# Kernel tuning notes

Hardware: AMD Instinct MI355X
Metric: run time of the kernel (lower is better)

The kernel has to match this reference:

```python
import jax, jax.numpy as jnp
import numpy as np

N_NODES = 100000
N_EDGES = 1600000
N_GRAPHS = 2048
D = 128
H = 128
EPS = 1e-5


def gcn_conv(x, src, dst, W, b, n):
    # x: [N, Din], W: [Din, Dout]; GCN with added self-loops and symmetric norm
    xw = x @ W                                       # [N, Dout]
    deg = jnp.zeros((n,), x.dtype).at[dst].add(1.0) + 1.0  # deg of A+I (counted on dst)
    dinv = jax.lax.rsqrt(deg)                        # [N]
    norm = dinv[src] * dinv[dst]                     # [E]
    msg = xw[src] * norm[:, None]                    # [E, Dout] gather + scale
    agg = jax.ops.segment_sum(msg, dst, num_segments=n)
    agg = agg + xw * (dinv * dinv)[:, None]          # self-loop contribution
    return agg + b


def gru_step_h0(x, W_ih, W_hh, b_ih, b_hh):
    # single GRU step with h0 = 0 (PyTorch gate order r, z, n)
    h0 = jnp.zeros_like(x)
    gi = x @ W_ih.T + b_ih                           # [G, 3H]
    gh = h0 @ W_hh.T + b_hh                          # [G, 3H] (zeros + b_hh)
    ir, iz, inn = jnp.split(gi, 3, axis=-1)
    hr, hz, hn = jnp.split(gh, 3, axis=-1)
    r = jax.nn.sigmoid(ir + hr)
    z = jax.nn.sigmoid(iz + hz)
    n = jnp.tanh(inn + r * hn)
    return (1.0 - z) * n + z * h0


def setup_inputs() -> dict:
    key = jax.random.key(0)
    ks = jax.random.split(key, 10)
    x = jax.random.normal(ks[0], (N_NODES, D), jnp.float32)
    edge_index = jax.random.randint(ks[1], (2, N_EDGES), 0, N_NODES, jnp.int32)
    batch = jnp.sort(jax.random.randint(ks[2], (N_NODES,), 0, N_GRAPHS, jnp.int32))
    s = 1.0 / np.sqrt(H)
    return {
        "x": x,
        "edge_index": edge_index,
        "batch": batch,
        "W1": jax.random.normal(ks[3], (D, H), jnp.float32) * s,
        "b1": jnp.zeros((H,), jnp.float32),
        "W2": jax.random.normal(ks[4], (H, H), jnp.float32) * s,
        "b2": jnp.zeros((H,), jnp.float32),
        "W_ih": jax.random.normal(ks[5], (3 * H, H), jnp.float32) * s,
        "W_hh": jax.random.normal(ks[6], (3 * H, H), jnp.float32) * s,
        "b_ih": jnp.zeros((3 * H,), jnp.float32),
        "b_hh": jnp.zeros((3 * H,), jnp.float32),
        "W_lin": jax.random.normal(ks[7], (1, H), jnp.float32) * s,
        "b_lin": jnp.zeros((1,), jnp.float32),
    }


def reference(x, edge_index, batch, W1, b1, W2, b2, W_ih, W_hh, b_ih, b_hh, W_lin, b_lin):
    src, dst = edge_index[0], edge_index[1]
    n = x.shape[0]
    h = jax.nn.relu(gcn_conv(x, src, dst, W1, b1, n))
    h = gcn_conv(h, src, dst, W2, b2, n)
    # global_mean_pool over graph ids
    sums = jax.ops.segment_sum(h, batch, num_segments=N_GRAPHS)
    cnts = jax.ops.segment_sum(jnp.ones((n,), h.dtype), batch, num_segments=N_GRAPHS)
    g = sums / jnp.maximum(cnts, 1.0)[:, None]       # [G, H]
    # dropout p=0.5 in eval mode -> identity
    g = gru_step_h0(g, W_ih, W_hh, b_ih, b_hh)
    g = jax.nn.relu(g)
    mu = jnp.mean(g, axis=-1, keepdims=True)
    var = jnp.mean(jnp.square(g - mu), axis=-1, keepdims=True)
    g = (g - mu) * jax.lax.rsqrt(var + EPS)          # layer_norm, no affine
    return g @ W_lin.T + b_lin                       # [G, 1]
```

## Files before the change

kernel.cpp:

```cpp
#include <hip/hip_runtime.h>
#include <hip/hip_bf16.h>
#include <math.h>

#define DHID 128
#define SH 8
#define BIN_T 8192
#define CAPSH 13
#define SRC_SH 13

typedef __attribute__((ext_vector_type(8))) short bf16x8;
typedef __attribute__((ext_vector_type(4))) float f32x4;

__device__ __forceinline__ int atomAddI(int* p, int v) {
    return __hip_atomic_fetch_add(p, v, __ATOMIC_RELAXED, __HIP_MEMORY_SCOPE_AGENT);
}
__device__ __forceinline__ float bf_lo(unsigned u) { return __uint_as_float(u << 16); }
__device__ __forceinline__ float bf_hi(unsigned u) { return __uint_as_float(u & 0xffff0000u); }
__device__ __forceinline__ float bf_us(unsigned short u) { return __uint_as_float((unsigned)u << 16); }
__device__ __forceinline__ unsigned short bf16_1(float f) {
    unsigned u = __float_as_uint(f);
    u += 0x7fffu + ((u >> 16) & 1u);
    return (unsigned short)(u >> 16);
}
__device__ __forceinline__ unsigned pack_bf16x2(float a, float b) {
    unsigned ua = __float_as_uint(a);
    unsigned ub = __float_as_uint(b);
    ua = (ua + 0x7fffu + ((ua >> 16) & 1u)) >> 16;
    ub = (ub + 0x7fffu + ((ub >> 16) & 1u)) & 0xffff0000u;
    return ua | ub;
}

__global__ __launch_bounds__(256) void bin_edges(const int* __restrict__ src,
                                                 const int* __restrict__ dst,
                                                 int* __restrict__ bcur,
                                                 unsigned* __restrict__ staged,
                                                 const float* __restrict__ W1,
                                                 const float* __restrict__ W2,
                                                 const float* __restrict__ Wih,
                                                 unsigned short* __restrict__ Wt1,
                                                 unsigned short* __restrict__ Wt2,
                                                 unsigned short* __restrict__ Wihb,
                                                 int E, int NB, int nb_bin) {
    int t = threadIdx.x;
    if (blockIdx.x >= nb_bin) {
        int idx = (blockIdx.x - nb_bin) * 256 + t;
        if (idx < 16384) {
            int k = idx >> 7, n = idx & 127;
            Wt1[n * 128 + k] = bf16_1(W1[idx]);
        } else if (idx < 32768) {
            int j = idx - 16384;
            int k = j >> 7, n = j & 127;
            Wt2[n * 128 + k] = bf16_1(W2[j]);
        } else if (idx < 32768 + 49152) {
            int j = idx - 32768;
            Wihb[j] = bf16_1(Wih[j]);
        }
        return;
    }
    __shared__ int lh[512], lbase[512], lcur[512];
    int e0 = blockIdx.x * BIN_T;
    int eend = min(e0 + BIN_T, E);
    for (int i = t; i < NB; i += 256) { lh[i] = 0; lcur[i] = 0; }
    __syncthreads();
    for (int e = e0 + t; e < eend; e += 256)
        atomicAdd(&lh[dst[e] >> SH], 1);
    __syncthreads();
    for (int i = t; i < NB; i += 256)
        lbase[i] = lh[i] ? atomAddI(&bcur[i], lh[i]) : 0;
    __syncthreads();
    for (int e = e0 + t; e < eend; e += 256) {
        int d = dst[e];
        int b = d >> SH;
        int pos = lbase[b] + atomicAdd(&lcur[b], 1);
        staged[((size_t)b << CAPSH) + pos] =
            (unsigned)src[e] | ((unsigned)(d & ((1 << SH) - 1)) << 24);
    }
}

__global__ __launch_bounds__(256) void scatter_csr(const unsigned* __restrict__ staged,
                                                   const int* __restrict__ bcur,
                                                   int* __restrict__ off,
                                                   float* __restrict__ dinv,
                                                   int* __restrict__ rec,
                                                   int N, int E, int NB) {
    __shared__ int hist[4096];
    __shared__ int sh[256];
    int t = threadIdx.x;
    int b = blockIdx.x;
    int node0 = b << SH;

    int s0 = (t < b) ? bcur[t] : 0;
    int s1 = (256 + t < b) ? bcur[256 + t] : 0;
    int s = s0 + s1;
#pragma unroll
    for (int o = 1; o < 64; o <<= 1) s += __shfl_xor(s, o);
    if ((t & 63) == 0) sh[t >> 6] = s;
    __syncthreads();
    int base = sh[0] + sh[1] + sh[2] + sh[3];
    __syncthreads();

    for (int i = t; i < 4096; i += 256) hist[i] = 0;
    __syncthreads();
    int cnt_b = bcur[b];
    const unsigned* st = staged + ((size_t)b << CAPSH);
    for (int j = t; j < cnt_b; j += 256) {
        unsigned w = st[j];
        int key = (int)((w >> 24) << 4) | (int)((w & 0xFFFFFFu) >> SRC_SH);
        atomicAdd(&hist[key], 1);
    }
    __syncthreads();

    int loc[16];
    int run = 0;
    int base16 = t * 16;
#pragma unroll
    for (int i = 0; i < 16; i++) { loc[i] = run; run += hist[base16 + i]; }
    sh[t] = run;
    __syncthreads();
#pragma unroll
    for (int o = 1; o < 256; o <<= 1) {
        int x = (t >= o) ? sh[t - o] : 0;
        __syncthreads();
        sh[t] += x;
        __syncthreads();
    }
    int excl = sh[t] - run;
#pragma unroll
    for (int i = 0; i < 16; i++) hist[base16 + i] = base + excl + loc[i];

    int node = node0 + t;
    if (node < N) {
        off[node] = base + excl;
        dinv[node] = rsqrtf((float)run + 1.0f);
    }
    if (b == NB - 1 && t == 0) off[N] = E;
    __syncthreads();

    for (int j = t; j < cnt_b; j += 256) {
        unsigned w = st[j];
        int key = (int)((w >> 24) << 4) | (int)((w & 0xFFFFFFu) >> SRC_SH);
        int pos = atomicAdd(&hist[key], 1);
        rec[pos] = (int)(w & 0xFFFFFFu);
    }
}

__global__ __launch_bounds__(256) void gemm_mfma(const void* __restrict__ Xv,
                                                 const unsigned short* __restrict__ Wt,
                                                 unsigned short* __restrict__ Y,
                                                 int N, int x_is_bf16,
                                                 int wstride, int ystride) {
    __shared__ unsigned short Xs[64 * 136];
    __shared__ unsigned short Ws[128 * 136];
    const int tid = threadIdx.x;
    const unsigned short* Wg = Wt + (size_t)blockIdx.y * wstride;
    unsigned short* Yg = Y + (size_t)blockIdx.y * ystride;

    {
        const uint4* W4 = (const uint4*)Wg;
#pragma unroll
        for (int i = 0; i < 8; i++) {
            int idx = tid + i * 256;
            int r = idx >> 4, c8 = idx & 15;
            *(uint4*)&Ws[r * 136 + c8 * 8] = W4[idx];
        }
    }
    const int row0 = blockIdx.x * 64;
    if (x_is_bf16) {
        const uint4* X4 = (const uint4*)Xv;
#pragma unroll
        for (int i = 0; i < 4; i++) {
            int idx = tid + i * 256;
            int r = idx >> 4, c8 = idx & 15;
            uint4 v = make_uint4(0u, 0u, 0u, 0u);
            if (row0 + r < N) v = X4[(size_t)(row0 + r) * 16 + c8];
            *(uint4*)&Xs[r * 136 + c8 * 8] = v;
        }
    } else {
        const float4* X4 = (const float4*)Xv;
#pragma unroll
        for (int i = 0; i < 8; i++) {
            int idx = tid + i * 256;
            int r = idx >> 5, c4 = idx & 31;
            float4 v = make_float4(0.f, 0.f, 0.f, 0.f);
            if (row0 + r < N) v = X4[(size_t)(row0 + r) * 32 + c4];
            uint2 pk = make_uint2(pack_bf16x2(v.x, v.y), pack_bf16x2(v.z, v.w));
            *(uint2*)&Xs[r * 136 + c4 * 4] = pk;
        }
    }
    __syncthreads();

    const int lane = tid & 63;
    const int wv = tid >> 6;
    const int m = lane & 15, quad = lane >> 4;
    const int wrow = wv * 16;

    f32x4 acc[8];
#pragma unroll
    for (int i = 0; i < 8; i++) acc[i] = (f32x4){0.f, 0.f, 0.f, 0.f};

#pragma unroll
    for (int kc = 0; kc < 4; kc++) {
        bf16x8 a = *(const bf16x8*)&Xs[(wrow + m) * 136 + kc * 32 + quad * 8];
#pragma unroll
        for (int nt = 0; nt < 8; nt++) {
            bf16x8 b = *(const bf16x8*)&Ws[(nt * 16 + m) * 136 + kc * 32 + quad * 8];
            acc[nt] = __builtin_amdgcn_mfma_f32_16x16x32_bf16(a, b, acc[nt], 0, 0, 0);
        }
    }

#pragma unroll
    for (int r = 0; r < 4; r++) {
        int lrow = wrow + quad * 4 + r;
#pragma unroll
        for (int nt = 0; nt < 8; nt++)
            Xs[lrow * 136 + nt * 16 + m] = bf16_1(acc[nt][r]);
    }
    __syncthreads();
#pragma unroll
    for (int i = 0; i < 4; i++) {
        int idx = tid + i * 256;
        int r = idx >> 4, c8 = idx & 15;
        if (row0 + r < N)
            *(uint4*)&Yg[(size_t)(row0 + r) * DHID + c8 * 8] =
                *(const uint4*)&Xs[r * 136 + c8 * 8];
    }
}

__global__ __launch_bounds__(256) void aggregate(const unsigned short* __restrict__ A,
                                                 const float* __restrict__ dinv,
                                                 const int* __restrict__ off,
                                                 const int* __restrict__ rec,
                                                 const float* __restrict__ bias,
                                                 unsigned short* __restrict__ Bout,
                                                 int N, int mode) {
    int node = blockIdx.x * 4 + (threadIdx.x >> 6);
    if (node >= N) return;
    int lane = threadIdx.x & 63;
    int q  = lane >> 4;
    int ql = lane & 15;
    float di = dinv[node];
    float2 acc[4];
    if (q == 0) {
        float s = di * di;
        uint4 v = ((const uint4*)(A + (size_t)node * DHID))[ql];
        const float4* bb = (const float4*)(bias + ql * 8);
        float4 b0 = bb[0], b1 = bb[1];
        acc[0] = make_float2(bf_lo(v.x) * s + b0.x, bf_hi(v.x) * s + b0.y);
        acc[1] = make_float2(bf_lo(v.y) * s + b0.z, bf_hi(v.y) * s + b0.w);
        acc[2] = make_float2(bf_lo(v.z) * s + b1.x, bf_hi(v.z) * s + b1.y);
        acc[3] = make_float2(bf_lo(v.w) * s + b1.z, bf_hi(v.w) * s + b1.w);
    } else {
#pragma unroll
        for (int i = 0; i < 4; i++) acc[i] = make_float2(0.f, 0.f);
    }
    int j = off[node] + q;
    int jend = off[node + 1];
    if (j + 4 < jend) {
        int s0 = rec[j], s1 = rec[j + 4];
        for (; j + 12 < jend; j += 8) {
            int n0 = rec[j + 8], n1 = rec[j + 12];
            uint4 v0 = ((const uint4*)(A + (size_t)s0 * DHID))[ql];
            uint4 v1 = ((const uint4*)(A + (size_t)s1 * DHID))[ql];
            float w0 = dinv[s0] * di;
            float w1 = dinv[s1] * di;
            acc[0].x += bf_lo(v0.x) * w0 + bf_lo(v1.x) * w1;
            acc[0].y += bf_hi(v0.x) * w0 + bf_hi(v1.x) * w1;
            acc[1].x += bf_lo(v0.y) * w0 + bf_lo(v1.y) * w1;
            acc[1].y += bf_hi(v0.y) * w0 + bf_hi(v1.y) * w1;
            acc[2].x += bf_lo(v0.z) * w0 + bf_lo(v1.z) * w1;
            acc[2].y += bf_hi(v0.z) * w0 + bf_hi(v1.z) * w1;
            acc[3].x += bf_lo(v0.w) * w0 + bf_lo(v1.w) * w1;
            acc[3].y += bf_hi(v0.w) * w0 + bf_hi(v1.w) * w1;
            s0 = n0; s1 = n1;
        }
        {
            uint4 v0 = ((const uint4*)(A + (size_t)s0 * DHID))[ql];
            uint4 v1 = ((const uint4*)(A + (size_t)s1 * DHID))[ql];
            float w0 = dinv[s0] * di;
            float w1 = dinv[s1] * di;
            acc[0].x += bf_lo(v0.x) * w0 + bf_lo(v1.x) * w1;
            acc[0].y += bf_hi(v0.x) * w0 + bf_hi(v1.x) * w1;
            acc[1].x += bf_lo(v0.y) * w0 + bf_lo(v1.y) * w1;
            acc[1].y += bf_hi(v0.y) * w0 + bf_hi(v1.y) * w1;
            acc[2].x += bf_lo(v0.z) * w0 + bf_lo(v1.z) * w1;
            acc[2].y += bf_hi(v0.z) * w0 + bf_hi(v1.z) * w1;
            acc[3].x += bf_lo(v0.w) * w0 + bf_lo(v1.w) * w1;
            acc[3].y += bf_hi(v0.w) * w0 + bf_hi(v1.w) * w1;
            j += 8;
        }
    }
    if (j < jend) {
        int s0 = rec[j];
        uint4 v0 = ((const uint4*)(A + (size_t)s0 * DHID))[ql];
        float w0 = dinv[s0] * di;
        acc[0].x += bf_lo(v0.x) * w0;
        acc[0].y += bf_hi(v0.x) * w0;
        acc[1].x += bf_lo(v0.y) * w0;
        acc[1].y += bf_hi(v0.y) * w0;
        acc[2].x += bf_lo(v0.z) * w0;
        acc[2].y += bf_hi(v0.z) * w0;
        acc[3].x += bf_lo(v0.w) * w0;
        acc[3].y += bf_hi(v0.w) * w0;
    }
#pragma unroll
    for (int i = 0; i < 4; i++) {
        acc[i].x += __shfl_xor(acc[i].x, 16);
        acc[i].y += __shfl_xor(acc[i].y, 16);
        acc[i].x += __shfl_xor(acc[i].x, 32);
        acc[i].y += __shfl_xor(acc[i].y, 32);
    }
    if (q == 0) {
        if (mode == 1) {
#pragma unroll
            for (int i = 0; i < 4; i++) {
                acc[i].x = fmaxf(acc[i].x, 0.f);
                acc[i].y = fmaxf(acc[i].y, 0.f);
            }
        }
        uint4 pk;
        pk.x = pack_bf16x2(acc[0].x, acc[0].y);
        pk.y = pack_bf16x2(acc[1].x, acc[1].y);
        pk.z = pack_bf16x2(acc[2].x, acc[2].y);
        pk.w = pack_bf16x2(acc[3].x, acc[3].y);
        ((uint4*)(Bout + (size_t)node * DHID))[ql] = pk;
    }
}

__global__ __launch_bounds__(256) void pool_mean(const unsigned short* __restrict__ B,
                                                 const int* __restrict__ batch,
                                                 float* __restrict__ g, int N, int G) {
    __shared__ int se[2];
    __shared__ float red[128];
    const int t = threadIdx.x;
    const int gr = blockIdx.x;
    if (t < 2) {
        int target = gr + t, lo = 0, hi = N;
        while (lo < hi) {
            int mid = (lo + hi) >> 1;
            if (batch[mid] < target) lo = mid + 1; else hi = mid;
        }
        se[t] = lo;
    }
    __syncthreads();
    const int s = se[0], e = se[1];
    const int col = t & 127, rh = t >> 7;
    float sum = 0.f;
    for (int r = s + rh; r < e; r += 2) sum += bf_us(B[(size_t)r * DHID + col]);
    if (rh == 1) red[col] = sum;
    __syncthreads();
    if (rh == 0) {
        float tot = sum + red[col];
        g[(size_t)gr * DHID + col] = tot / fmaxf((float)(e - s), 1.0f);
    }
}

__global__ __launch_bounds__(128) void gate_ln_head(const unsigned short* __restrict__ gi,
                                                    const float* __restrict__ b_ih,
                                                    const float* __restrict__ b_hh,
                                                    const float* __restrict__ W_lin,
                                                    const float* __restrict__ b_lin,
                                                    float* __restrict__ out, int G) {
    __shared__ float red[2];
    const int t = threadIdx.x;
    const int g = blockIdx.x;

    float d0 = bf_us(gi[(size_t)g * DHID + t]);
    float d1 = bf_us(gi[(size_t)(G + g) * DHID + t]);
    float d2 = bf_us(gi[(size_t)(2 * G + g) * DHID + t]);

    float rg = 1.f / (1.f + expf(-(d0 + b_ih[t] + b_hh[t])));
    float zg = 1.f / (1.f + expf(-(d1 + b_ih[128 + t] + b_hh[128 + t])));
    float ng = tanhf(d2 + b_ih[256 + t] + rg * b_hh[256 + t]);
    float y = fmaxf((1.f - zg) * ng, 0.f);

    auto blockSum = [&](float v) -> float {
#pragma unroll
        for (int o = 1; o < 64; o <<= 1) v += __shfl_xor(v, o);
        __syncthreads();
        if ((t & 63) == 0) red[t >> 6] = v;
        __syncthreads();
        return red[0] + red[1];
    };

    float mu = blockSum(y) * (1.f / 128.f);
    float dy = y - mu;
    float var = blockSum(dy * dy) * (1.f / 128.f);
    float yn = dy * rsqrtf(var + 1e-5f);
    float tot = blockSum(yn * W_lin[t]);
    if (t == 0) out[g] = tot + b_lin[0];
}

extern "C" void kernel_launch(void* const* d_in, const int* in_sizes, int n_in,
                              void* d_out, int out_size, void* d_ws, size_t ws_size,
                              hipStream_t stream) {
    const float* x     = (const float*)d_in[0];
    const int*   ei    = (const int*)d_in[1];
    const int*   batch = (const int*)d_in[2];
    const float* W1    = (const float*)d_in[3];
    const float* b1    = (const float*)d_in[4];
    const float* W2    = (const float*)d_in[5];
    const float* b2    = (const float*)d_in[6];
    const float* W_ih  = (const float*)d_in[7];
    const float* b_ih  = (const float*)d_in[9];
    const float* b_hh  = (const float*)d_in[10];
    const float* W_lin = (const float*)d_in[11];
    const float* b_lin = (const float*)d_in[12];
    float* out = (float*)d_out;

    const int N = in_sizes[0] / DHID;
    const int E = in_sizes[1] / 2;
    const int G = out_size;
    const int* src = ei;
    const int* dst = ei + E;
    const int NB = (N + (1 << SH) - 1) >> SH;

    auto align256 = [](size_t v) { return (v + 255) & ~(size_t)255; };
    char* p = (char*)d_ws;
    size_t used = 0;
    auto carve = [&](size_t bytes) -> char* {
        char* q = p + used;
        used += align256(bytes);
        return q;
    };

    int*   off    = (int*)carve(((size_t)N + 1) * 4);
    int*   bcur   = (int*)carve(512 * 4);
    float* dinv   = (float*)carve((size_t)N * 4);
    unsigned* staged = (unsigned*)carve(((size_t)NB << CAPSH) * 4);
    int*   rec    = (int*)carve((size_t)E * 4);
    float* gbuf   = (float*)carve((size_t)G * DHID * 4);
    unsigned short* Wt1  = (unsigned short*)carve((size_t)128 * 128 * 2);
    unsigned short* Wt2  = (unsigned short*)carve((size_t)128 * 128 * 2);
    unsigned short* Wihb = (unsigned short*)carve((size_t)3 * 128 * 128 * 2);
    unsigned short* gib  = (unsigned short*)carve((size_t)3 * G * DHID * 2);
    unsigned short* A    = (unsigned short*)carve((size_t)N * DHID * 2);
    unsigned short* B1b  = (unsigned short*)carve((size_t)N * DHID * 2);
    size_t matB = (size_t)N * DHID * 2;
    unsigned short* B2b;
    if (ws_size >= used + matB) {
        B2b = (unsigned short*)carve(matB);
    } else {
        B2b = (unsigned short*)d_in[0];
    }

    dim3 blk(256);
    int nb_g  = (N + 63) / 64;
    int nb_ag = (N + 3) / 4;
    int nb_bin = (E + BIN_T - 1) / BIN_T;
    int nb_wp  = (81920 + 255) / 256;

    hipMemsetAsync(bcur, 0, (size_t)NB * 4, stream);
    bin_edges<<<nb_bin + nb_wp, blk, 0, stream>>>(src, dst, bcur, staged,
                                                  W1, W2, W_ih, Wt1, Wt2, Wihb,
                                                  E, NB, nb_bin);
    scatter_csr<<<NB, blk, 0, stream>>>(staged, bcur, off, dinv, rec, N, E, NB);

    gemm_mfma<<<dim3(nb_g, 1), blk, 0, stream>>>(x, Wt1, A, N, 0, 0, 0);
    aggregate<<<nb_ag, blk, 0, stream>>>(A, dinv, off, rec, b1, B1b, N, 1);

    gemm_mfma<<<dim3(nb_g, 1), blk, 0, stream>>>(B1b, Wt2, A, N, 1, 0, 0);
    aggregate<<<nb_ag, blk, 0, stream>>>(A, dinv, off, rec, b2, B2b, N, 0);

    pool_mean<<<G, blk, 0, stream>>>(B2b, batch, gbuf, N, G);
    gemm_mfma<<<dim3((G + 63) / 64, 3), blk, 0, stream>>>(gbuf, Wihb, gib, G, 0,
                                                          128 * 128, G * DHID);
    gate_ln_head<<<G, dim3(128), 0, stream>>>(gib, b_ih, b_hh, W_lin, b_lin, out, G);
}
```

Baseline: 348.7 us.

## Merge CSR scatter with first GEMM into one launch; deepen aggregate gather unroll

Folds the CSR scatter blocks and the first-layer x@W1 GEMM blocks into a single kernel, branching on block index, so both independent stages run concurrently and one launch is removed. The aggregate kernel's edge loop now issues four row gathers per iteration instead of a software-pipelined pair, giving more memory-level parallelism. The fused kernel carries the larger of the two shared-memory footprints (about 51 KB) for every block, which may limit occupancy for the scatter blocks. The wider unroll also raises register use in aggregate.

Measured after the change: 336.8 us. -3.4%, faster.

```diff
diff --git a/kernel.cpp b/kernel.cpp
--- a/kernel.cpp
+++ b/kernel.cpp
@@ -77,152 +77,139 @@
     }
 }
 
-__global__ __launch_bounds__(256) void scatter_csr(const unsigned* __restrict__ staged,
-                                                   const int* __restrict__ bcur,
-                                                   int* __restrict__ off,
-                                                   float* __restrict__ dinv,
-                                                   int* __restrict__ rec,
-                                                   int N, int E, int NB) {
-    __shared__ int hist[4096];
-    __shared__ int sh[256];
-    int t = threadIdx.x;
-    int b = blockIdx.x;
-    int node0 = b << SH;
-
-    int s0 = (t < b) ? bcur[t] : 0;
-    int s1 = (256 + t < b) ? bcur[256 + t] : 0;
-    int s = s0 + s1;
-#pragma unroll
-    for (int o = 1; o < 64; o <<= 1) s += __shfl_xor(s, o);
-    if ((t & 63) == 0) sh[t >> 6] = s;
-    __syncthreads();
-    int base = sh[0] + sh[1] + sh[2] + sh[3];
-    __syncthreads();
-
-    for (int i = t; i < 4096; i += 256) hist[i] = 0;
-    __syncthreads();
-    int cnt_b = bcur[b];
-    const unsigned* st = staged + ((size_t)b << CAPSH);
-    for (int j = t; j < cnt_b; j += 256) {
-        unsigned w = st[j];
-        int key = (int)((w >> 24) << 4) | (int)((w & 0xFFFFFFu) >> SRC_SH);
-        atomicAdd(&hist[key], 1);
-    }
-    __syncthreads();
-
-    int loc[16];
-    int run = 0;
-    int base16 = t * 16;
-#pragma unroll
-    for (int i = 0; i < 16; i++) { loc[i] = run; run += hist[base16 + i]; }
-    sh[t] = run;
-    __syncthreads();
-#pragma unroll
-    for (int o = 1; o < 256; o <<= 1) {
-        int x = (t >= o) ? sh[t - o] : 0;
-        __syncthreads();
-        sh[t] += x;
-        __syncthreads();
-    }
-    int excl = sh[t] - run;
-#pragma unroll
-    for (int i = 0; i < 16; i++) hist[base16 + i] = base + excl + loc[i];
-
-    int node = node0 + t;
-    if (node < N) {
-        off[node] = base + excl;
-        dinv[node] = rsqrtf((float)run + 1.0f);
-    }
-    if (b == NB - 1 && t == 0) off[N] = E;
-    __syncthreads();
-
-    for (int j = t; j < cnt_b; j += 256) {
-        unsigned w = st[j];
-        int key = (int)((w >> 24) << 4) | (int)((w & 0xFFFFFFu) >> SRC_SH);
-        int pos = atomicAdd(&hist[key], 1);
-        rec[pos] = (int)(w & 0xFFFFFFu);
-    }
-}
-
-__global__ __launch_bounds__(256) void gemm_mfma(const void* __restrict__ Xv,
-                                                 const unsigned short* __restrict__ Wt,
-                                                 unsigned short* __restrict__ Y,
-                                                 int N, int x_is_bf16,
-                                                 int wstride, int ystride) {
-    __shared__ unsigned short Xs[64 * 136];
-    __shared__ unsigned short Ws[128 * 136];
+__global__ __launch_bounds__(256) void scatter_gemm(const unsigned* __restrict__ staged,
+                                                    const int* __restrict__ bcur,
+                                                    int* __restrict__ off,
+                                                    float* __restrict__ dinv,
+                                                    int* __restrict__ rec,
+                                                    int N, int E, int NB,
+                                                    const float* __restrict__ Xf,
+                                                    const unsigned short* __restrict__ Wt,
+                                                    unsigned short* __restrict__ Y) {
+    __shared__ __align__(16) unsigned char smem[52224];
     const int tid = threadIdx.x;
-    const unsigned short* Wg = Wt + (size_t)blockIdx.y * wstride;
-    unsigned short* Yg = Y + (size_t)blockIdx.y * ystride;
-
-    {
-        const uint4* W4 = (const uint4*)Wg;
-#pragma unroll
-        for (int i = 0; i < 8; i++) {
-            int idx = tid + i * 256;
-            int r = idx >> 4, c8 = idx & 15;
-            *(uint4*)&Ws[r * 136 + c8 * 8] = W4[idx];
-        }
-    }
-    const int row0 = blockIdx.x * 64;
-    if (x_is_bf16) {
-        const uint4* X4 = (const uint4*)Xv;
+    if (blockIdx.x < NB) {
+        int* hist = (int*)smem;
+        int* sh   = (int*)(smem + 16384);
+        int t = tid;
+        int b = blockIdx.x;
+        int node0 = b << SH;
+
+        int s0 = (t < b) ? bcur[t] : 0;
+        int s1 = (256 + t < b) ? bcur[256 + t] : 0;
+        int s = s0 + s1;
+#pragma unroll
+        for (int o = 1; o < 64; o <<= 1) s += __shfl_xor(s, o);
+        if ((t & 63) == 0) sh[t >> 6] = s;
+        __syncthreads();
+        int base = sh[0] + sh[1] + sh[2] + sh[3];
+        __syncthreads();
+
+        for (int i = t; i < 4096; i += 256) hist[i] = 0;
+        __syncthreads();
+        int cnt_b = bcur[b];
+        const unsigned* st = staged + ((size_t)b << CAPSH);
+        for (int j = t; j < cnt_b; j += 256) {
+            unsigned w = st[j];
+            int key = (int)((w >> 24) << 4) | (int)((w & 0xFFFFFFu) >> SRC_SH);
+            atomicAdd(&hist[key], 1);
+        }
+        __syncthreads();
+
+        int loc[16];
+        int run = 0;
+        int base16 = t * 16;
+#pragma unroll
+        for (int i = 0; i < 16; i++) { loc[i] = run; run += hist[base16 + i]; }
+        sh[t] = run;
+        __syncthreads();
+#pragma unroll
+        for (int o = 1; o < 256; o <<= 1) {
+            int x = (t >= o) ? sh[t - o] : 0;
+            __syncthreads();
+            sh[t] += x;
+            __syncthreads();
+        }
+        int excl = sh[t] - run;
+#pragma unroll
+        for (int i = 0; i < 16; i++) hist[base16 + i] = base + excl + loc[i];
+
+        int node = node0 + t;
+        if (node < N) {
+            off[node] = base + excl;
+            dinv[node] = rsqrtf((float)run + 1.0f);
+        }
+        if (b == NB - 1 && t == 0) off[N] = E;
+        __syncthreads();
+
+        for (int j = t; j < cnt_b; j += 256) {
+            unsigned w = st[j];
+            int key = (int)((w >> 24) << 4) | (int)((w & 0xFFFFFFu) >> SRC_SH);
+            int pos = atomicAdd(&hist[key], 1);
+            rec[pos] = (int)(w & 0xFFFFFFu);
+        }
+    } else {
+        unsigned short* Xs = (unsigned short*)smem;
+        unsigned short* Ws = (unsigned short*)(smem + 17408);
+        {
+            const uint4* W4 = (const uint4*)Wt;
+#pragma unroll
+            for (int i = 0; i < 8; i++) {
+                int idx = tid + i * 256;
+                int r = idx >> 4, c8 = idx & 15;
+                *(uint4*)&Ws[r * 136 + c8 * 8] = W4[idx];
+            }
+        }
+        const int row0 = (blockIdx.x - NB) * 64;
+        {
+            const float4* X4 = (const float4*)Xf;
+#pragma unroll
+            for (int i = 0; i < 8; i++) {
+                int idx = tid + i * 256;
+                int r = idx >> 5, c4 = idx & 31;
+                float4 v = make_float4(0.f, 0.f, 0.f, 0.f);
+                if (row0 + r < N) v = X4[(size_t)(row0 + r) * 32 + c4];
+                uint2 pk = make_uint2(pack_bf16x2(v.x, v.y), pack_bf16x2(v.z, v.w));
+                *(uint2*)&Xs[r * 136 + c4 * 4] = pk;
+            }
+        }
+        __syncthreads();
+
+        const int lane = tid & 63;
+        const int wv = tid >> 6;
+        const int m = lane & 15, quad = lane >> 4;
+        const int wrow = wv * 16;
+
+        f32x4 acc[8];
+#pragma unroll
+        for (int i = 0; i < 8; i++) acc[i] = (f32x4){0.f, 0.f, 0.f, 0.f};
+
+#pragma unroll
+        for (int kc = 0; kc < 4; kc++) {
+            bf16x8 a = *(const bf16x8*)&Xs[(wrow + m) * 136 + kc * 32 + quad * 8];
+#pragma unroll
+            for (int nt = 0; nt < 8; nt++) {
+                bf16x8 bfr = *(const bf16x8*)&Ws[(nt * 16 + m) * 136 + kc * 32 + quad * 8];
+                acc[nt] = __builtin_amdgcn_mfma_f32_16x16x32_bf16(a, bfr, acc[nt], 0, 0, 0);
+            }
+        }
+
+#pragma unroll
+        for (int r = 0; r < 4; r++) {
+            int lrow = wrow + quad * 4 + r;
+#pragma unroll
+            for (int nt = 0; nt < 8; nt++)
+                Xs[lrow * 136 + nt * 16 + m] = bf16_1(acc[nt][r]);
+        }
+        __syncthreads();
 #pragma unroll
         for (int i = 0; i < 4; i++) {
             int idx = tid + i * 256;
             int r = idx >> 4, c8 = idx & 15;
-            uint4 v = make_uint4(0u, 0u, 0u, 0u);
-            if (row0 + r < N) v = X4[(size_t)(row0 + r) * 16 + c8];
-            *(uint4*)&Xs[r * 136 + c8 * 8] = v;
-        }
-    } else {
-        const float4* X4 = (const float4*)Xv;
-#pragma unroll
-        for (int i = 0; i < 8; i++) {
-            int idx = tid + i * 256;
-            int r = idx >> 5, c4 = idx & 31;
-            float4 v = make_float4(0.f, 0.f, 0.f, 0.f);
-            if (row0 + r < N) v = X4[(size_t)(row0 + r) * 32 + c4];
-            uint2 pk = make_uint2(pack_bf16x2(v.x, v.y), pack_bf16x2(v.z, v.w));
-            *(uint2*)&Xs[r * 136 + c4 * 4] = pk;
-        }
-    }
-    __syncthreads();
-
-    const int lane = tid & 63;
-    const int wv = tid >> 6;
-    const int m = lane & 15, quad = lane >> 4;
-    const int wrow = wv * 16;
-
-    f32x4 acc[8];
-#pragma unroll
-    for (int i = 0; i < 8; i++) acc[i] = (f32x4){0.f, 0.f, 0.f, 0.f};
-
-#pragma unroll
-    for (int kc = 0; kc < 4; kc++) {
-        bf16x8 a = *(const bf16x8*)&Xs[(wrow + m) * 136 + kc * 32 + quad * 8];
-#pragma unroll
-        for (int nt = 0; nt < 8; nt++) {
-            bf16x8 b = *(const bf16x8*)&Ws[(nt * 16 + m) * 136 + kc * 32 + quad * 8];
-            acc[nt] = __builtin_amdgcn_mfma_f32_16x16x32_bf16(a, b, acc[nt], 0, 0, 0);
-        }
-    }
-
-#pragma unroll
-    for (int r = 0; r < 4; r++) {
-        int lrow = wrow + quad * 4 + r;
-#pragma unroll
-        for (int nt = 0; nt < 8; nt++)
-            Xs[lrow * 136 + nt * 16 + m] = bf16_1(acc[nt][r]);
-    }
-    __syncthreads();
-#pragma unroll
-    for (int i = 0; i < 4; i++) {
-        int idx = tid + i * 256;
-        int r = idx >> 4, c8 = idx & 15;
-        if (row0 + r < N)
-            *(uint4*)&Yg[(size_t)(row0 + r) * DHID + c8 * 8] =
-                *(const uint4*)&Xs[r * 136 + c8 * 8];
+            if (row0 + r < N)
+                *(uint4*)&Y[(size_t)(row0 + r) * DHID + c8 * 8] =
+                    *(const uint4*)&Xs[r * 136 + c8 * 8];
+        }
     }
 }
 
@@ -255,39 +242,39 @@
     }
     int j = off[node] + q;
     int jend = off[node + 1];
-    if (j + 4 < jend) {
+    for (; j + 12 < jend; j += 16) {
+        int s0 = rec[j], s1 = rec[j + 4], s2 = rec[j + 8], s3 = rec[j + 12];
+        uint4 v0 = ((const uint4*)(A + (size_t)s0 * DHID))[ql];
+        uint4 v1 = ((const uint4*)(A + (size_t)s1 * DHID))[ql];
+        uint4 v2 = ((const uint4*)(A + (size_t)s2 * DHID))[ql];
+        uint4 v3 = ((const uint4*)(A + (size_t)s3 * DHID))[ql];
+        float w0 = dinv[s0] * di;
+        float w1 = dinv[s1] * di;
+        float w2 = dinv[s2] * di;
+        float w3 = dinv[s3] * di;
+        acc[0].x += bf_lo(v0.x) * w0 + bf_lo(v1.x) * w1 + bf_lo(v2.x) * w2 + bf_lo(v3.x) * w3;
+        acc[0].y += bf_hi(v0.x) * w0 + bf_hi(v1.x) * w1 + bf_hi(v2.x) * w2 + bf_hi(v3.x) * w3;
+        acc[1].x += bf_lo(v0.y) * w0 + bf_lo(v1.y) * w1 + bf_lo(v2.y) * w2 + bf_lo(v3.y) * w3;
+        acc[1].y += bf_hi(v0.y) * w0 + bf_hi(v1.y) * w1 + bf_hi(v2.y) * w2 + bf_hi(v3.y) * w3;
+        acc[2].x += bf_lo(v0.z) * w0 + bf_lo(v1.z) * w1 + bf_lo(v2.z) * w2 + bf_lo(v3.z) * w3;
+        acc[2].y += bf_hi(v0.z) * w0 + bf_hi(v1.z) * w1 + bf_hi(v2.z) * w2 + bf_hi(v3.z) * w3;
+        acc[3].x += bf_lo(v0.w) * w0 + bf_lo(v1.w) * w1 + bf_lo(v2.w) * w2 + bf_lo(v3.w) * w3;
+        acc[3].y += bf_hi(v0.w) * w0 + bf_hi(v1.w) * w1 + bf_hi(v2.w) * w2 + bf_hi(v3.w) * w3;
+    }
+    for (; j + 4 < jend; j += 8) {
         int s0 = rec[j], s1 = rec[j + 4];
-        for (; j + 12 < jend; j += 8) {
-            int n0 = rec[j + 8], n1 = rec[j + 12];
-            uint4 v0 = ((const uint4*)(A + (size_t)s0 * DHID))[ql];
-            uint4 v1 = ((const uint4*)(A + (size_t)s1 * DHID))[ql];
-            float w0 = dinv[s0] * di;
-            float w1 = dinv[s1] * di;
-            acc[0].x += bf_lo(v0.x) * w0 + bf_lo(v1.x) * w1;
-            acc[0].y += bf_hi(v0.x) * w0 + bf_hi(v1.x) * w1;
-            acc[1].x += bf_lo(v0.y) * w0 + bf_lo(v1.y) * w1;
-            acc[1].y += bf_hi(v0.y) * w0 + bf_hi(v1.y) * w1;
-            acc[2].x += bf_lo(v0.z) * w0 + bf_lo(v1.z) * w1;
-            acc[2].y += bf_hi(v0.z) * w0 + bf_hi(v1.z) * w1;
-            acc[3].x += bf_lo(v0.w) * w0 + bf_lo(v1.w) * w1;
-            acc[3].y += bf_hi(v0.w) * w0 + bf_hi(v1.w) * w1;
-            s0 = n0; s1 = n1;
-        }
-        {
-            uint4 v0 = ((const uint4*)(A + (size_t)s0 * DHID))[ql];
-            uint4 v1 = ((const uint4*)(A + (size_t)s1 * DHID))[ql];
-            float w0 = dinv[s0] * di;
-            float w1 = dinv[s1] * di;
-            acc[0].x += bf_lo(v0.x) * w0 + bf_lo(v1.x) * w1;
-            acc[0].y += bf_hi(v0.x) * w0 + bf_hi(v1.x) * w1;
-            acc[1].x += bf_lo(v0.y) * w0 + bf_lo(v1.y) * w1;
-            acc[1].y += bf_hi(v0.y) * w0 + bf_hi(v1.y) * w1;
-            acc[2].x += bf_lo(v0.z) * w0 + bf_lo(v1.z) * w1;
-            acc[2].y += bf_hi(v0.z) * w0 + bf_hi(v1.z) * w1;
-            acc[3].x += bf_lo(v0.w) * w0 + bf_lo(v1.w) * w1;
-            acc[3].y += bf_hi(v0.w) * w0 + bf_hi(v1.w) * w1;
-            j += 8;
-        }
+        uint4 v0 = ((const uint4*)(A + (size_t)s0 * DHID))[ql];
+        uint4 v1 = ((const uint4*)(A + (size_t)s1 * DHID))[ql];
+        float w0 = dinv[s0] * di;
+        float w1 = dinv[s1] * di;
+        acc[0].x += bf_lo(v0.x) * w0 + bf_lo(v1.x) * w1;
+        acc[0].y += bf_hi(v0.x) * w0 + bf_hi(v1.x) * w1;
+        acc[1].x += bf_lo(v0.y) * w0 + bf_lo(v1.y) * w1;
+        acc[1].y += bf_hi(v0.y) * w0 + bf_hi(v1.y) * w1;
+        acc[2].x += bf_lo(v0.z) * w0 + bf_lo(v1.z) * w1;
+        acc[2].y += bf_hi(v0.z) * w0 + bf_hi(v1.z) * w1;
+        acc[3].x += bf_lo(v0.w) * w0 + bf_lo(v1.w) * w1;
+        acc[3].y += bf_hi(v0.w) * w0 + bf_hi(v1.w) * w1;
     }
     if (j < jend) {
         int s0 = rec[j];
@@ -323,6 +310,88 @@
         pk.z = pack_bf16x2(acc[2].x, acc[2].y);
         pk.w = pack_bf16x2(acc[3].x, acc[3].y);
         ((uint4*)(Bout + (size_t)node * DHID))[ql] = pk;
+    }
+}
+
+__global__ __launch_bounds__(256) void gemm_mfma(const void* __restrict__ Xv,
+                                                 const unsigned short* __restrict__ Wt,
+                                                 unsigned short* __restrict__ Y,
+                                                 int N, int x_is_bf16,
+                                                 int wstride, int ystride) {
+    __shared__ unsigned short Xs[64 * 136];
+    __shared__ unsigned short Ws[128 * 136];
+    const int tid = threadIdx.x;
+    const unsigned short* Wg = Wt + (size_t)blockIdx.y * wstride;
+    unsigned short* Yg = Y + (size_t)blockIdx.y * ystride;
+
+    {
+        const uint4* W4 = (const uint4*)Wg;
+#pragma unroll
+        for (int i = 0; i < 8; i++) {
+            int idx = tid + i * 256;
+            int r = idx >> 4, c8 = idx & 15;
+            *(uint4*)&Ws[r * 136 + c8 * 8] = W4[idx];
+        }
+    }
+    const int row0 = blockIdx.x * 64;
+    if (x_is_bf16) {
+        const uint4* X4 = (const uint4*)Xv;
+#pragma unroll
+        for (int i = 0; i < 4; i++) {
+            int idx = tid + i * 256;
+            int r = idx >> 4, c8 = idx & 15;
+            uint4 v = make_uint4(0u, 0u, 0u, 0u);
+            if (row0 + r < N) v = X4[(size_t)(row0 + r) * 16 + c8];
+            *(uint4*)&Xs[r * 136 + c8 * 8] = v;
+        }
+    } else {
+        const float4* X4 = (const float4*)Xv;
+#pragma unroll
+        for (int i = 0; i < 8; i++) {
+            int idx = tid + i * 256;
+            int r = idx >> 5, c4 = idx & 31;
+            float4 v = make_float4(0.f, 0.f, 0.f, 0.f);
+            if (row0 + r < N) v = X4[(size_t)(row0 + r) * 32 + c4];
+            uint2 pk = make_uint2(pack_bf16x2(v.x, v.y), pack_bf16x2(v.z, v.w));
+            *(uint2*)&Xs[r * 136 + c4 * 4] = pk;
+        }
+    }
+    __syncthreads();
+
+    const int lane = tid & 63;
+    const int wv = tid >> 6;
+    const int m = lane & 15, quad = lane >> 4;
+    const int wrow = wv * 16;
+
+    f32x4 acc[8];
+#pragma unroll
+    for (int i = 0; i < 8; i++) acc[i] = (f32x4){0.f, 0.f, 0.f, 0.f};
+
+#pragma unroll
+    for (int kc = 0; kc < 4; kc++) {
+        bf16x8 a = *(const bf16x8*)&Xs[(wrow + m) * 136 + kc * 32 + quad * 8];
+#pragma unroll
+        for (int nt = 0; nt < 8; nt++) {
+            bf16x8 b = *(const bf16x8*)&Ws[(nt * 16 + m) * 136 + kc * 32 + quad * 8];
+            acc[nt] = __builtin_amdgcn_mfma_f32_16x16x32_bf16(a, b, acc[nt], 0, 0, 0);
+        }
+    }
+
+#pragma unroll
+    for (int r = 0; r < 4; r++) {
+        int lrow = wrow + quad * 4 + r;
+#pragma unroll
+        for (int nt = 0; nt < 8; nt++)
+            Xs[lrow * 136 + nt * 16 + m] = bf16_1(acc[nt][r]);
+    }
+    __syncthreads();
+#pragma unroll
+    for (int i = 0; i < 4; i++) {
+        int idx = tid + i * 256;
+        int r = idx >> 4, c8 = idx & 15;
+        if (row0 + r < N)
+            *(uint4*)&Yg[(size_t)(row0 + r) * DHID + c8 * 8] =
+                *(const uint4*)&Xs[r * 136 + c8 * 8];
     }
 }
 
@@ -453,9 +522,9 @@
     bin_edges<<<nb_bin + nb_wp, blk, 0, stream>>>(src, dst, bcur, staged,
                                                   W1, W2, W_ih, Wt1, Wt2, Wihb,
                                                   E, NB, nb_bin);
-    scatter_csr<<<NB, blk, 0, stream>>>(staged, bcur, off, dinv, rec, N, E, NB);
-
-    gemm_mfma<<<dim3(nb_g, 1), blk, 0, stream>>>(x, Wt1, A, N, 0, 0, 0);
+    scatter_gemm<<<NB + nb_g, blk, 0, stream>>>(staged, bcur, off, dinv, rec,
+                                                N, E, NB, x, Wt1, A);
+
     aggregate<<<nb_ag, blk, 0, stream>>>(A, dinv, off, rec, b1, B1b, N, 1);
 
     gemm_mfma<<<dim3(nb_g, 1), blk, 0, stream>>>(B1b, Wt2, A, N, 1, 0, 0);
```
